# Performance work log

Measured on AMD Instinct MI355X. Metric: run time of the kernel, lower is better.

The kernel has to match this reference:

```python
import jax, jax.numpy as jnp
import numpy as np

B = 2048          # num_graphs
N_PER = 68        # landmarks per graph
DEG = 8           # avg degree -> 544 edges per graph
E_PER = N_PER * DEG
F_IN, F_HID, N_CLUST = 2, 128, 8


def setup_inputs() -> dict:
    key = jax.random.key(0)
    ks = jax.random.split(key, 16)
    N = B * N_PER
    x = jax.random.normal(ks[0], (N, F_IN), dtype=jnp.float32)
    # intra-graph random edges: local ids in [0,68) + per-graph offset
    local = jax.random.randint(ks[1], (2, B, E_PER), 0, N_PER)
    offs = (jnp.arange(B, dtype=jnp.int64) * N_PER)[None, :, None]
    edge_index = (local.astype(jnp.int64) + offs).reshape(2, -1)
    adj = jax.random.uniform(ks[2], (B, N_PER, N_PER), dtype=jnp.float32)
    s = jax.random.normal(ks[3], (B, N_PER, N_CLUST), dtype=jnp.float32)
    def lin(k, fi, fo):
        return jax.random.normal(k, (fi, fo), dtype=jnp.float32) / np.sqrt(fi)
    return {
        'x': x, 'edge_index': edge_index, 'adj': adj, 's': s,
        'W_root1': lin(ks[4], F_IN, F_HID), 'W_rel1': lin(ks[5], F_IN, F_HID),
        'b1': jnp.zeros((F_HID,), jnp.float32),
        'W_root2': lin(ks[6], F_HID, F_HID), 'W_rel2': lin(ks[7], F_HID, F_HID),
        'b2': jnp.zeros((F_HID,), jnp.float32),
        'W_root3': lin(ks[8], F_HID, F_HID), 'W_rel3': lin(ks[9], F_HID, F_HID),
        'b3': jnp.zeros((F_HID,), jnp.float32),
        'fc_w': lin(ks[10], F_HID, 1), 'fc_b': jnp.zeros((1,), jnp.float32),
    }


def _graph_conv(x, src, dst, W_root, W_rel, b, num_nodes):
    # PyG GraphConv (aggr='add'): out_i = W_rel @ sum_{j->i} x_j + W_root @ x_i + b
    agg = jax.ops.segment_sum(x[src], dst, num_segments=num_nodes)
    return agg @ W_rel + x @ W_root + b


def reference(x, edge_index, adj, s,
              W_root1, W_rel1, b1, W_root2, W_rel2, b2,
              W_root3, W_rel3, b3, fc_w, fc_b):
    N = x.shape[0]
    src, dst = edge_index[0], edge_index[1]
    h = jax.nn.relu(_graph_conv(x, src, dst, W_root1, W_rel1, b1, N))
    h = jax.nn.relu(_graph_conv(h, src, dst, W_root2, W_rel2, b2, N))
    h = jax.nn.relu(_graph_conv(h, src, dst, W_root3, W_rel3, b3, N))
    bsz = adj.shape[0]
    xr = h.reshape(bsz, N_PER, F_HID)            # [B,68,128]
    s_sm = jax.nn.softmax(s, axis=-1)            # dense_diff_pool softmax
    xp = jnp.einsum('bnc,bnf->bcf', s_sm, xr)    # pooled features [B,8,128]
    # (pooled adj / link / entropy losses are computed then discarded in the
    #  original forward; they do not affect the returned value -> omitted)
    # MaxPool2d((1,8)) over [B,8,128] -> [B,8,16]
    pooled = xp.reshape(bsz, N_CLUST, F_HID // 8, 8).max(axis=-1)
    flat = pooled.reshape(bsz, -1)               # [B,128]
    return flat @ fc_w + fc_b                    # [B,1]
```

## Files before the change

kernel.cpp:

```cpp
#include <hip/hip_runtime.h>
#include <hip/hip_bf16.h>

#define NPER 68
#define ROWP 80
#define EPER 544
#define FH   128
#define NC   8

typedef short short8 __attribute__((ext_vector_type(8)));
typedef short short4v __attribute__((ext_vector_type(4)));
typedef float f32x4 __attribute__((ext_vector_type(4)));

__device__ __forceinline__ unsigned short f2bf(float f) {
    unsigned int u = __float_as_uint(f);
    return (unsigned short)((u + 0x7FFFu + ((u >> 16) & 1u)) >> 16);
}
__device__ __forceinline__ float bf2f(unsigned short h) {
    return __uint_as_float(((unsigned int)h) << 16);
}
__device__ __forceinline__ unsigned int swz(unsigned int row, unsigned int bytecol) {
    return row * 512u + (bytecol ^ ((row & 7u) << 4));
}

__global__ void pack_w(const float* __restrict__ Wrel2, const float* __restrict__ Wroot2,
                       const float* __restrict__ Wrel3, const float* __restrict__ Wroot3,
                       unsigned short* __restrict__ ws) {
    int o = blockIdx.x * 256 + threadIdx.x;
    int j = o & 7, l = (o >> 3) & 63, n = (o >> 9) & 7, t = (o >> 12) & 7, L = o >> 15;
    int k = t * 32 + ((l >> 4) << 3) + j;
    int f = n * 16 + (l & 15);
    const float* Wl = L ? Wrel3 : Wrel2;
    const float* Wr = L ? Wroot3 : Wroot2;
    float v = (k < FH) ? Wl[k * FH + f] : Wr[(k - FH) * FH + f];
    ws[o] = f2bf(v);
}

__launch_bounds__(256, 3)
__global__ void gnn_kernel(const float* __restrict__ x,
                           const int*   __restrict__ ei,
                           const float* __restrict__ s,
                           const float* __restrict__ Wroot1, const float* __restrict__ Wrel1, const float* __restrict__ b1,
                           const float* __restrict__ b2, const float* __restrict__ b3,
                           const unsigned short* __restrict__ wpack,
                           const float* __restrict__ fcw, const float* __restrict__ fcb,
                           float* __restrict__ out, int nE)
{
    __shared__ __align__(16) unsigned short hcat[ROWP * 256];
    __shared__ unsigned short edst_t[EPER];
    __shared__ unsigned short esrc[EPER];
    __shared__ int   cnt[NPER];
    __shared__ int   coff[NPER + 1];
    __shared__ float xl[NPER][2];
    __shared__ float aggx[NPER][2];
    __shared__ float ssm[NPER][NC];
    __shared__ float xp[NC][FH];

    const int g     = blockIdx.x;
    const int tid   = threadIdx.x;
    const int lane  = tid & 63;
    const int wid   = tid >> 6;
    const int gnode = g * NPER;
    const int gedge = g * EPER;

    const int* srcp = ei;
    const int* dstp = ei + nE;

    if (tid < NPER) cnt[tid] = 0;
    for (int i = tid; i < NPER * 2; i += 256)
        ((float*)xl)[i] = x[gnode * 2 + i];
    for (int i = tid; i < (ROWP - NPER) * 128; i += 256)
        ((unsigned int*)(hcat + NPER * 256))[i] = 0u;
    __syncthreads();

    for (int e = tid; e < EPER; e += 256) {
        int gd = dstp[gedge + e] - gnode;
        edst_t[e] = (unsigned short)gd;
        atomicAdd(&cnt[gd], 1);
    }
    __syncthreads();
    if (tid == 0) {
        int acc = 0; coff[0] = 0;
        for (int i = 0; i < NPER; ++i) { acc += cnt[i]; coff[i + 1] = acc; }
    }
    __syncthreads();
    if (tid < NPER) cnt[tid] = coff[tid];
    __syncthreads();
    for (int e = tid; e < EPER; e += 256) {
        int gd  = edst_t[e];
        int pos = atomicAdd(&cnt[gd], 1);
        esrc[pos] = (unsigned short)(srcp[gedge + e] - gnode);
    }
    __syncthreads();

    for (int i = tid; i < NPER; i += 256) {
        float s0 = 0.f, s1 = 0.f;
        for (int e = coff[i]; e < coff[i + 1]; ++e) {
            int si = esrc[e];
            s0 += xl[si][0]; s1 += xl[si][1];
        }
        aggx[i][0] = s0; aggx[i][1] = s1;
    }
    __syncthreads();
    for (int idx = tid; idx < NPER * FH; idx += 256) {
        int i = idx >> 7, f = idx & 127;
        float v = b1[f]
                + aggx[i][0] * Wrel1[f]  + aggx[i][1] * Wrel1[FH + f]
                + xl[i][0]   * Wroot1[f] + xl[i][1]   * Wroot1[FH + f];
        v = v > 0.f ? v : 0.f;
        *(unsigned short*)((char*)hcat + swz(i, (128 + f) * 2)) = f2bf(v);
    }
    __syncthreads();

    #pragma unroll
    for (int L = 0; L < 2; ++L) {
        for (int idx = tid; idx < NPER * 16; idx += 256) {
            int i = idx >> 4, fg = idx & 15;
            float acc[8];
            #pragma unroll
            for (int j = 0; j < 8; ++j) acc[j] = 0.f;
            int e0 = coff[i], e1 = coff[i + 1];
            for (int e = e0; e < e1; ++e) {
                int src = esrc[e];
                short8 hv = *(const short8*)((char*)hcat + swz(src, 256 + fg * 16));
                #pragma unroll
                for (int j = 0; j < 8; ++j) acc[j] += bf2f((unsigned short)hv[j]);
            }
            short8 r;
            #pragma unroll
            for (int j = 0; j < 8; ++j) r[j] = (short)f2bf(acc[j]);
            *(short8*)((char*)hcat + swz(i, fg * 16)) = r;
        }
        __syncthreads();

        const unsigned short* wsL = wpack + (L << 15);
        f32x4 acc[5][2];
        #pragma unroll
        for (int m = 0; m < 5; ++m) { acc[m][0] = (f32x4)0.f; acc[m][1] = (f32x4)0.f; }
        const int arow = lane & 15, akoff = (lane >> 4) * 8;
        for (int t = 0; t < 8; ++t) {
            short8 bf0 = *(const short8*)(wsL + (((t * 8 + wid * 2 + 0) * 64 + lane) << 3));
            short8 bf1 = *(const short8*)(wsL + (((t * 8 + wid * 2 + 1) * 64 + lane) << 3));
            int k = t * 32 + akoff;
            #pragma unroll
            for (int m = 0; m < 5; ++m) {
                short8 a = *(const short8*)((char*)hcat + swz(m * 16 + arow, k * 2));
                acc[m][0] = __builtin_amdgcn_mfma_f32_16x16x32_bf16(a, bf0, acc[m][0], 0, 0, 0);
                acc[m][1] = __builtin_amdgcn_mfma_f32_16x16x32_bf16(a, bf1, acc[m][1], 0, 0, 0);
            }
        }
        __syncthreads();

        const float* bv = L ? b3 : b2;
        #pragma unroll
        for (int c2 = 0; c2 < 2; ++c2) {
            int f = (wid * 2 + c2) * 16 + (lane & 15);
            float bias = bv[f];
            #pragma unroll
            for (int m = 0; m < 5; ++m) {
                #pragma unroll
                for (int i2 = 0; i2 < 4; ++i2) {
                    int row = m * 16 + (lane >> 4) * 4 + i2;
                    float v = acc[m][c2][i2] + bias;
                    v = v > 0.f ? v : 0.f;
                    *(unsigned short*)((char*)hcat + swz(row, (128 + f) * 2)) = f2bf(v);
                }
            }
        }
        __syncthreads();
    }

    for (int i = tid; i < NPER; i += 256) {
        float v[NC]; float m = -1e30f;
        #pragma unroll
        for (int c = 0; c < NC; ++c) { v[c] = s[(gnode + i) * NC + c]; m = fmaxf(m, v[c]); }
        float sum = 0.f;
        #pragma unroll
        for (int c = 0; c < NC; ++c) { v[c] = __expf(v[c] - m); sum += v[c]; }
        float inv = 1.f / sum;
        #pragma unroll
        for (int c = 0; c < NC; ++c) ssm[i][c] = v[c] * inv;
    }
    __syncthreads();

    {
        int c = tid >> 5, fq = tid & 31;
        float a4[4] = {0.f, 0.f, 0.f, 0.f};
        for (int n = 0; n < NPER; ++n) {
            float sc = ssm[n][c];
            short4v hv = *(const short4v*)((char*)hcat + swz(n, 256 + fq * 8));
            #pragma unroll
            for (int j = 0; j < 4; ++j) a4[j] += sc * bf2f((unsigned short)hv[j]);
        }
        #pragma unroll
        for (int j = 0; j < 4; ++j) xp[c][fq * 4 + j] = a4[j];
    }
    __syncthreads();

    float partial = 0.f;
    if (tid < 128) {
        int c = tid >> 4, q = tid & 15;
        float m = xp[c][q * 8];
        #pragma unroll
        for (int j = 1; j < 8; ++j) m = fmaxf(m, xp[c][q * 8 + j]);
        partial = m * fcw[tid];
    }
    __syncthreads();
    float* red = &ssm[0][0];
    if (tid < 128) red[tid] = partial;
    __syncthreads();
    if (tid < 64) {
        float v = red[tid] + red[tid + 64];
        #pragma unroll
        for (int off = 32; off > 0; off >>= 1) v += __shfl_down(v, off, 64);
        if (tid == 0) out[g] = v + fcb[0];
    }
}

extern "C" void kernel_launch(void* const* d_in, const int* in_sizes, int n_in,
                              void* d_out, int out_size, void* d_ws, size_t ws_size,
                              hipStream_t stream) {
    const float* x      = (const float*)d_in[0];
    const int*   ei     = (const int*)d_in[1];
    const float* s      = (const float*)d_in[3];
    const float* Wroot1 = (const float*)d_in[4];
    const float* Wrel1  = (const float*)d_in[5];
    const float* b1     = (const float*)d_in[6];
    const float* Wroot2 = (const float*)d_in[7];
    const float* Wrel2  = (const float*)d_in[8];
    const float* b2     = (const float*)d_in[9];
    const float* Wroot3 = (const float*)d_in[10];
    const float* Wrel3  = (const float*)d_in[11];
    const float* b3     = (const float*)d_in[12];
    const float* fcw    = (const float*)d_in[13];
    const float* fcb    = (const float*)d_in[14];
    float* out = (float*)d_out;
    unsigned short* wpack = (unsigned short*)d_ws;

    const int nE = in_sizes[1] / 2;
    const int B  = in_sizes[3] / (NPER * NC);

    pack_w<<<256, 256, 0, stream>>>(Wrel2, Wroot2, Wrel3, Wroot3, wpack);
    gnn_kernel<<<B, 256, 0, stream>>>(x, ei, s,
                                      Wroot1, Wrel1, b1,
                                      b2, b3, wpack,
                                      fcw, fcb, out, nE);
}
```

Baseline: 207.7 us.

## Replace CSR edge aggregation with dense adjacency MFMA matmuls

```diff
diff --git a/kernel.cpp b/kernel.cpp
--- a/kernel.cpp
+++ b/kernel.cpp
@@ -6,9 +6,9 @@
 #define EPER 544
 #define FH   128
 #define NC   8
+#define ADJW 104
 
 typedef short short8 __attribute__((ext_vector_type(8)));
-typedef short short4v __attribute__((ext_vector_type(4)));
 typedef float f32x4 __attribute__((ext_vector_type(4)));
 
 __device__ __forceinline__ unsigned short f2bf(float f) {
@@ -18,8 +18,8 @@
 __device__ __forceinline__ float bf2f(unsigned short h) {
     return __uint_as_float(((unsigned int)h) << 16);
 }
-__device__ __forceinline__ unsigned int swz(unsigned int row, unsigned int bytecol) {
-    return row * 512u + (bytecol ^ ((row & 7u) << 4));
+__device__ __forceinline__ unsigned int swzB(unsigned int row, unsigned int bc) {
+    return row * 512u + (bc ^ (((row ^ (row >> 3)) & 7u) << 4));
 }
 
 __global__ void pack_w(const float* __restrict__ Wrel2, const float* __restrict__ Wroot2,
@@ -35,164 +35,208 @@
     ws[o] = f2bf(v);
 }
 
-__launch_bounds__(256, 3)
+__launch_bounds__(256, 2)
 __global__ void gnn_kernel(const float* __restrict__ x,
                            const int*   __restrict__ ei,
                            const float* __restrict__ s,
-                           const float* __restrict__ Wroot1, const float* __restrict__ Wrel1, const float* __restrict__ b1,
+                           const float* __restrict__ Wroot1, const float* __restrict__ Wrel1,
+                           const float* __restrict__ b1,
                            const float* __restrict__ b2, const float* __restrict__ b3,
                            const unsigned short* __restrict__ wpack,
                            const float* __restrict__ fcw, const float* __restrict__ fcb,
                            float* __restrict__ out, int nE)
 {
     __shared__ __align__(16) unsigned short hcat[ROWP * 256];
-    __shared__ unsigned short edst_t[EPER];
-    __shared__ unsigned short esrc[EPER];
-    __shared__ int   cnt[NPER];
-    __shared__ int   coff[NPER + 1];
+    __shared__ __align__(16) unsigned short adjb[ROWP * ADJW];
+    __shared__ __align__(16) unsigned short sT[16 * ADJW];
     __shared__ float xl[NPER][2];
-    __shared__ float aggx[NPER][2];
-    __shared__ float ssm[NPER][NC];
     __shared__ float xp[NC][FH];
-
-    const int g     = blockIdx.x;
-    const int tid   = threadIdx.x;
-    const int lane  = tid & 63;
-    const int wid   = tid >> 6;
-    const int gnode = g * NPER;
-    const int gedge = g * EPER;
-
+    __shared__ float red[128];
+
+    const int g = blockIdx.x, tid = threadIdx.x, lane = tid & 63, wid = tid >> 6;
+    const int gnode = g * NPER, gedge = g * EPER;
     const int* srcp = ei;
     const int* dstp = ei + nE;
-
-    if (tid < NPER) cnt[tid] = 0;
-    for (int i = tid; i < NPER * 2; i += 256)
-        ((float*)xl)[i] = x[gnode * 2 + i];
-    for (int i = tid; i < (ROWP - NPER) * 128; i += 256)
-        ((unsigned int*)(hcat + NPER * 256))[i] = 0u;
+    unsigned int* adj32 = (unsigned int*)adjb;
+    unsigned int* h32   = (unsigned int*)hcat;
+
+    for (int i = tid; i < (ROWP * ADJW) / 2; i += 256) adj32[i] = 0u;
+    for (int i = tid; i < (16 * ADJW) / 2; i += 256) ((unsigned int*)sT)[i] = 0u;
+    for (int i = tid; i < 12 * 128; i += 256) h32[NPER * 128 + i] = 0u;
+    for (int i = tid; i < NPER * 32; i += 256) h32[(i >> 5) * 128 + (i & 31)] = 0u;
+    for (int i = tid; i < NPER * 2; i += 256) ((float*)xl)[i] = x[gnode * 2 + i];
     __syncthreads();
 
     for (int e = tid; e < EPER; e += 256) {
-        int gd = dstp[gedge + e] - gnode;
-        edst_t[e] = (unsigned short)gd;
-        atomicAdd(&cnt[gd], 1);
-    }
-    __syncthreads();
-    if (tid == 0) {
-        int acc = 0; coff[0] = 0;
-        for (int i = 0; i < NPER; ++i) { acc += cnt[i]; coff[i + 1] = acc; }
-    }
-    __syncthreads();
-    if (tid < NPER) cnt[tid] = coff[tid];
-    __syncthreads();
-    for (int e = tid; e < EPER; e += 256) {
-        int gd  = edst_t[e];
-        int pos = atomicAdd(&cnt[gd], 1);
-        esrc[pos] = (unsigned short)(srcp[gedge + e] - gnode);
-    }
-    __syncthreads();
-
-    for (int i = tid; i < NPER; i += 256) {
-        float s0 = 0.f, s1 = 0.f;
-        for (int e = coff[i]; e < coff[i + 1]; ++e) {
-            int si = esrc[e];
-            s0 += xl[si][0]; s1 += xl[si][1];
-        }
-        aggx[i][0] = s0; aggx[i][1] = s1;
-    }
-    __syncthreads();
-    for (int idx = tid; idx < NPER * FH; idx += 256) {
-        int i = idx >> 7, f = idx & 127;
-        float v = b1[f]
-                + aggx[i][0] * Wrel1[f]  + aggx[i][1] * Wrel1[FH + f]
-                + xl[i][0]   * Wroot1[f] + xl[i][1]   * Wroot1[FH + f];
-        v = v > 0.f ? v : 0.f;
-        *(unsigned short*)((char*)hcat + swz(i, (128 + f) * 2)) = f2bf(v);
-    }
-    __syncthreads();
-
-    #pragma unroll
+        int s_ = srcp[gedge + e] - gnode;
+        int d_ = dstp[gedge + e] - gnode;
+        int idx = d_ * ADJW + s_;
+        atomicAdd(&adj32[idx >> 1], (idx & 1) ? 0x10000u : 1u);
+    }
+    __syncthreads();
+    for (int i = tid; i < (ROWP * ADJW) / 2; i += 256) {
+        unsigned int u = adj32[i];
+        if (u) {
+            adj32[i] = (unsigned int)f2bf((float)(u & 0xffffu))
+                     | ((unsigned int)f2bf((float)(u >> 16)) << 16);
+        }
+    }
+    __syncthreads();
+
+    if (tid < 136) {
+        int i = tid >> 1, ft = tid & 1;
+        float a = 0.f;
+        for (int j = 0; j < NPER; ++j) a += bf2f(adjb[i * ADJW + j]) * xl[j][ft];
+        *(unsigned short*)((char*)hcat + swzB(i, ft * 2))     = f2bf(a);
+        *(unsigned short*)((char*)hcat + swzB(i, 4 + ft * 2)) = f2bf(xl[i][ft]);
+    } else if (tid < 204) {
+        int i = tid - 136;
+        float v[NC]; float m = -1e30f;
+        #pragma unroll
+        for (int c = 0; c < NC; ++c) { v[c] = s[(gnode + i) * NC + c]; m = fmaxf(m, v[c]); }
+        float sum = 0.f;
+        #pragma unroll
+        for (int c = 0; c < NC; ++c) { v[c] = __expf(v[c] - m); sum += v[c]; }
+        float inv = 1.f / sum;
+        #pragma unroll
+        for (int c = 0; c < NC; ++c) sT[c * ADJW + i] = f2bf(v[c] * inv);
+    }
+    __syncthreads();
+
+    const int arow = lane & 15, aq = lane >> 4, akB = aq * 16;
+
+    auto epilogue_h = [&](f32x4 (&acc)[5][2], const float* __restrict__ bv) {
+        #pragma unroll
+        for (int c2 = 0; c2 < 2; ++c2) {
+            int f = (wid * 2 + c2) * 16 + arow;
+            float bias = bv[f];
+            #pragma unroll
+            for (int m = 0; m < 5; ++m)
+                #pragma unroll
+                for (int i2 = 0; i2 < 4; ++i2) {
+                    int row = m * 16 + aq * 4 + i2;
+                    if (row < NPER) {
+                        float v = acc[m][c2][i2] + bias;
+                        v = v > 0.f ? v : 0.f;
+                        *(unsigned short*)((char*)hcat + swzB(row, (FH + f) * 2)) = f2bf(v);
+                    }
+                }
+        }
+    };
+
+    {
+        f32x4 acc[5][2];
+        #pragma unroll
+        for (int m = 0; m < 5; ++m) { acc[m][0] = (f32x4)0.f; acc[m][1] = (f32x4)0.f; }
+        short8 bf[2];
+        #pragma unroll
+        for (int c2 = 0; c2 < 2; ++c2) {
+            int f = (wid * 2 + c2) * 16 + arow;
+            #pragma unroll
+            for (int j = 0; j < 8; ++j) {
+                float wv = 0.f;
+                if (aq == 0) {
+                    if (j < 2) wv = Wrel1[j * FH + f];
+                    else if (j < 4) wv = Wroot1[(j - 2) * FH + f];
+                }
+                bf[c2][j] = (short)f2bf(wv);
+            }
+        }
+        #pragma unroll
+        for (int m = 0; m < 5; ++m) {
+            short8 a = *(const short8*)((char*)hcat + swzB(m * 16 + arow, akB));
+            acc[m][0] = __builtin_amdgcn_mfma_f32_16x16x32_bf16(a, bf[0], acc[m][0], 0, 0, 0);
+            acc[m][1] = __builtin_amdgcn_mfma_f32_16x16x32_bf16(a, bf[1], acc[m][1], 0, 0, 0);
+        }
+        epilogue_h(acc, b1);
+    }
+    __syncthreads();
+
+    #pragma unroll 1
     for (int L = 0; L < 2; ++L) {
-        for (int idx = tid; idx < NPER * 16; idx += 256) {
-            int i = idx >> 4, fg = idx & 15;
-            float acc[8];
-            #pragma unroll
-            for (int j = 0; j < 8; ++j) acc[j] = 0.f;
-            int e0 = coff[i], e1 = coff[i + 1];
-            for (int e = e0; e < e1; ++e) {
-                int src = esrc[e];
-                short8 hv = *(const short8*)((char*)hcat + swz(src, 256 + fg * 16));
-                #pragma unroll
-                for (int j = 0; j < 8; ++j) acc[j] += bf2f((unsigned short)hv[j]);
-            }
-            short8 r;
-            #pragma unroll
-            for (int j = 0; j < 8; ++j) r[j] = (short)f2bf(acc[j]);
-            *(short8*)((char*)hcat + swz(i, fg * 16)) = r;
+        f32x4 acc[5][2];
+        #pragma unroll
+        for (int m = 0; m < 5; ++m) { acc[m][0] = (f32x4)0.f; acc[m][1] = (f32x4)0.f; }
+        for (int kt = 0; kt < 3; ++kt) {
+            short8 bg[2];
+            #pragma unroll
+            for (int c2 = 0; c2 < 2; ++c2) {
+                int f = (wid * 2 + c2) * 16 + arow;
+                unsigned int cb = (FH + f) * 2;
+                #pragma unroll
+                for (int j = 0; j < 8; ++j) {
+                    int k = kt * 32 + aq * 8 + j;
+                    int r = k < ROWP ? k : 0;
+                    bg[c2][j] = (short)*(const unsigned short*)((char*)hcat + swzB(r, cb));
+                }
+            }
+            #pragma unroll
+            for (int m = 0; m < 5; ++m) {
+                short8 a = *(const short8*)((char*)adjb + (m * 16 + arow) * (ADJW * 2) + kt * 64 + akB);
+                acc[m][0] = __builtin_amdgcn_mfma_f32_16x16x32_bf16(a, bg[0], acc[m][0], 0, 0, 0);
+                acc[m][1] = __builtin_amdgcn_mfma_f32_16x16x32_bf16(a, bg[1], acc[m][1], 0, 0, 0);
+            }
+        }
+        #pragma unroll
+        for (int c2 = 0; c2 < 2; ++c2) {
+            int f = (wid * 2 + c2) * 16 + arow;
+            #pragma unroll
+            for (int m = 0; m < 5; ++m)
+                #pragma unroll
+                for (int i2 = 0; i2 < 4; ++i2) {
+                    int row = m * 16 + aq * 4 + i2;
+                    if (row < NPER)
+                        *(unsigned short*)((char*)hcat + swzB(row, f * 2)) = f2bf(acc[m][c2][i2]);
+                }
         }
         __syncthreads();
 
+        f32x4 acc2[5][2];
+        #pragma unroll
+        for (int m = 0; m < 5; ++m) { acc2[m][0] = (f32x4)0.f; acc2[m][1] = (f32x4)0.f; }
         const unsigned short* wsL = wpack + (L << 15);
-        f32x4 acc[5][2];
-        #pragma unroll
-        for (int m = 0; m < 5; ++m) { acc[m][0] = (f32x4)0.f; acc[m][1] = (f32x4)0.f; }
-        const int arow = lane & 15, akoff = (lane >> 4) * 8;
         for (int t = 0; t < 8; ++t) {
             short8 bf0 = *(const short8*)(wsL + (((t * 8 + wid * 2 + 0) * 64 + lane) << 3));
             short8 bf1 = *(const short8*)(wsL + (((t * 8 + wid * 2 + 1) * 64 + lane) << 3));
-            int k = t * 32 + akoff;
             #pragma unroll
             for (int m = 0; m < 5; ++m) {
-                short8 a = *(const short8*)((char*)hcat + swz(m * 16 + arow, k * 2));
-                acc[m][0] = __builtin_amdgcn_mfma_f32_16x16x32_bf16(a, bf0, acc[m][0], 0, 0, 0);
-                acc[m][1] = __builtin_amdgcn_mfma_f32_16x16x32_bf16(a, bf1, acc[m][1], 0, 0, 0);
+                short8 a = *(const short8*)((char*)hcat + swzB(m * 16 + arow, t * 64 + akB));
+                acc2[m][0] = __builtin_amdgcn_mfma_f32_16x16x32_bf16(a, bf0, acc2[m][0], 0, 0, 0);
+                acc2[m][1] = __builtin_amdgcn_mfma_f32_16x16x32_bf16(a, bf1, acc2[m][1], 0, 0, 0);
             }
         }
         __syncthreads();
-
-        const float* bv = L ? b3 : b2;
-        #pragma unroll
-        for (int c2 = 0; c2 < 2; ++c2) {
-            int f = (wid * 2 + c2) * 16 + (lane & 15);
-            float bias = bv[f];
-            #pragma unroll
-            for (int m = 0; m < 5; ++m) {
-                #pragma unroll
-                for (int i2 = 0; i2 < 4; ++i2) {
-                    int row = m * 16 + (lane >> 4) * 4 + i2;
-                    float v = acc[m][c2][i2] + bias;
-                    v = v > 0.f ? v : 0.f;
-                    *(unsigned short*)((char*)hcat + swz(row, (128 + f) * 2)) = f2bf(v);
-                }
-            }
-        }
+        epilogue_h(acc2, L ? b3 : b2);
         __syncthreads();
     }
 
-    for (int i = tid; i < NPER; i += 256) {
-        float v[NC]; float m = -1e30f;
-        #pragma unroll
-        for (int c = 0; c < NC; ++c) { v[c] = s[(gnode + i) * NC + c]; m = fmaxf(m, v[c]); }
-        float sum = 0.f;
-        #pragma unroll
-        for (int c = 0; c < NC; ++c) { v[c] = __expf(v[c] - m); sum += v[c]; }
-        float inv = 1.f / sum;
-        #pragma unroll
-        for (int c = 0; c < NC; ++c) ssm[i][c] = v[c] * inv;
-    }
-    __syncthreads();
-
     {
-        int c = tid >> 5, fq = tid & 31;
-        float a4[4] = {0.f, 0.f, 0.f, 0.f};
-        for (int n = 0; n < NPER; ++n) {
-            float sc = ssm[n][c];
-            short4v hv = *(const short4v*)((char*)hcat + swz(n, 256 + fq * 8));
-            #pragma unroll
-            for (int j = 0; j < 4; ++j) a4[j] += sc * bf2f((unsigned short)hv[j]);
-        }
-        #pragma unroll
-        for (int j = 0; j < 4; ++j) xp[c][fq * 4 + j] = a4[j];
+        f32x4 accp[2]; accp[0] = (f32x4)0.f; accp[1] = (f32x4)0.f;
+        for (int kt = 0; kt < 3; ++kt) {
+            short8 bg[2];
+            #pragma unroll
+            for (int c2 = 0; c2 < 2; ++c2) {
+                int f = (wid * 2 + c2) * 16 + arow;
+                unsigned int cb = (FH + f) * 2;
+                #pragma unroll
+                for (int j = 0; j < 8; ++j) {
+                    int k = kt * 32 + aq * 8 + j;
+                    int r = k < ROWP ? k : 0;
+                    bg[c2][j] = (short)*(const unsigned short*)((char*)hcat + swzB(r, cb));
+                }
+            }
+            short8 a = *(const short8*)(sT + arow * ADJW + kt * 32 + aq * 8);
+            accp[0] = __builtin_amdgcn_mfma_f32_16x16x32_bf16(a, bg[0], accp[0], 0, 0, 0);
+            accp[1] = __builtin_amdgcn_mfma_f32_16x16x32_bf16(a, bg[1], accp[1], 0, 0, 0);
+        }
+        #pragma unroll
+        for (int c2 = 0; c2 < 2; ++c2) {
+            int f = (wid * 2 + c2) * 16 + arow;
+            if (aq < 2) {
+                #pragma unroll
+                for (int i2 = 0; i2 < 4; ++i2) xp[aq * 4 + i2][f] = accp[c2][i2];
+            }
+        }
     }
     __syncthreads();
 
@@ -204,8 +248,6 @@
         for (int j = 1; j < 8; ++j) m = fmaxf(m, xp[c][q * 8 + j]);
         partial = m * fcw[tid];
     }
-    __syncthreads();
-    float* red = &ssm[0][0];
     if (tid < 128) red[tid] = partial;
     __syncthreads();
     if (tid < 64) {
```

Result: faster. 186.8 us (-10.1%).
